# Performance work log

Measured on AMD Instinct MI355X. Metric: run time of the kernel, lower is better.

The kernel has to match this reference:

```python
import jax, jax.numpy as jnp
import numpy as np

N, IN_SZ, OUT_SZ = 8192, 512, 64

def setup_inputs() -> dict:
    key = jax.random.key(0)
    ks = jax.random.split(key, 7)
    s_in = 1.0 / np.sqrt(IN_SZ)
    inp = {
        "input": jax.random.normal(ks[0], (N, IN_SZ), dtype=jnp.float32),
        "Wq": jax.random.uniform(ks[1], (OUT_SZ, IN_SZ), jnp.float32, -s_in, s_in),
        "bq": jax.random.uniform(ks[2], (OUT_SZ,), jnp.float32, -s_in, s_in),
        "Wk": jax.random.uniform(ks[3], (OUT_SZ, IN_SZ), jnp.float32, -s_in, s_in),
        "bk": jax.random.uniform(ks[4], (OUT_SZ,), jnp.float32, -s_in, s_in),
        "Wv": jax.random.uniform(ks[5], (OUT_SZ, IN_SZ), jnp.float32, -s_in, s_in),
        "bv": jax.random.uniform(ks[6], (OUT_SZ,), jnp.float32, -s_in, s_in),
    }
    return inp

def reference(input, Wq, bq, Wk, bk, Wv, bv):
    # torch nn.Linear: x @ W.T + b
    q = input @ Wq.T + bq  # [N, out]
    k = input @ Wk.T + bk  # [N, out]
    v = input @ Wv.T + bv  # [N, out]
    # NOTE: original module has NO 1/sqrt(d) scaling.
    scores = jax.nn.softmax(q @ k.T, axis=-1)  # [N, N]
    return scores @ v  # [N, out]
```

## Files before the change

kernel.cpp:

```cpp
#include <hip/hip_runtime.h>
#include <math.h>

#define SA_N   8192
#define SA_IN  512
#define SA_D   64
#define G_SPL  16

typedef short s16x8 __attribute__((ext_vector_type(8)));
typedef float f32x16 __attribute__((ext_vector_type(16)));

#define MFMA32(A, B, C) __builtin_amdgcn_mfma_f32_32x32x16_bf16((A), (B), (C), 0, 0, 0)

static __device__ __forceinline__ unsigned short f2bf_rn(float x) {
    unsigned int u = __float_as_uint(x);
    unsigned int r = (u + 0x7FFFu + ((u >> 16) & 1u)) >> 16;
    return (unsigned short)r;
}

static __device__ __forceinline__ void trunc_split(float f, unsigned short* hi, unsigned short* lo) {
    unsigned int u = __float_as_uint(f);
    *hi = (unsigned short)(u >> 16);
    float lf = f - __uint_as_float(u & 0xFFFF0000u);
    *lo = (unsigned short)(__float_as_uint(lf) >> 16);
}

static __device__ __forceinline__ void split8(const float4 a, const float4 b, s16x8* xh, s16x8* xl) {
    union { unsigned int u[4]; s16x8 v; } H, L;
    const float f[8] = {a.x, a.y, a.z, a.w, b.x, b.y, b.z, b.w};
#pragma unroll
    for (int p = 0; p < 4; ++p) {
        const unsigned int u0 = __float_as_uint(f[2 * p]);
        const unsigned int u1 = __float_as_uint(f[2 * p + 1]);
        H.u[p] = (u0 >> 16) | (u1 & 0xFFFF0000u);
        const float l0 = f[2 * p]     - __uint_as_float(u0 & 0xFFFF0000u);
        const float l1 = f[2 * p + 1] - __uint_as_float(u1 & 0xFFFF0000u);
        L.u[p] = (__float_as_uint(l0) >> 16) | (__float_as_uint(l1) & 0xFFFF0000u);
    }
    *xh = H.v; *xl = L.v;
}

static __device__ __forceinline__ s16x8 pack_rn8(const float4 a, const float4 b) {
    union { unsigned int u[4]; s16x8 v; } P;
    const float f[8] = {a.x, a.y, a.z, a.w, b.x, b.y, b.z, b.w};
#pragma unroll
    for (int p = 0; p < 4; ++p)
        P.u[p] = (unsigned int)f2bf_rn(f[2 * p]) | ((unsigned int)f2bf_rn(f[2 * p + 1]) << 16);
    return P.v;
}

__global__ __launch_bounds__(256, 2) void qkv_kernel(
    const float* __restrict__ in,
    const float* __restrict__ Wq, const float* __restrict__ bq,
    const float* __restrict__ Wk, const float* __restrict__ bk,
    const float* __restrict__ Wv, const float* __restrict__ bv,
    unsigned short* __restrict__ Qhi, unsigned short* __restrict__ Qlo,
    unsigned short* __restrict__ KhiF, unsigned short* __restrict__ KloF,
    unsigned short* __restrict__ VF)
{
    __shared__ float cbuf[2][4][64][20];
    __shared__ __align__(16) unsigned short stage[4096];
    const int t    = threadIdx.x;
    const int w    = t >> 6;
    const int lane = t & 63;
    const int h    = lane >> 5;
    const int q32  = lane & 31;
    const int mat  = blockIdx.x >> 8;
    const int jt   = blockIdx.x & 255;
    const int rows0 = jt * 32;

    const float* W = (mat == 0) ? Wq : (mat == 1 ? Wk : Wv);
    const float* B = (mat == 0) ? bq : (mat == 1 ? bk : bv);

    f32x16 accA[2] = {};
    f32x16 accB[2] = {};

#pragma unroll 2
    for (int ksl = 0; ksl < 8; ++ksl) {
        const int ks = (w << 3) + ksl;
        const float* xp = in + (size_t)(rows0 + q32) * SA_IN + ks * 16 + h * 8;
        const float4 xa = *(const float4*)xp;
        const float4 xb = *(const float4*)(xp + 4);
        s16x8 xh, xl;
        split8(xa, xb, &xh, &xl);
#pragma unroll
        for (int mt = 0; mt < 2; ++mt) {
            const float* wp = W + (size_t)(mt * 32 + q32) * SA_IN + ks * 16 + h * 8;
            const float4 wa = *(const float4*)wp;
            const float4 wb = *(const float4*)(wp + 4);
            if (mat < 2) {
                s16x8 ah, al;
                split8(wa, wb, &ah, &al);
                accA[mt] = MFMA32(ah, xh, accA[mt]);
                accB[mt] = MFMA32(ah, xl, accB[mt]);
                accA[mt] = MFMA32(al, xh, accA[mt]);
            } else {
                const s16x8 ah = pack_rn8(wa, wb);
                accA[mt] = MFMA32(ah, xh, accA[mt]);
            }
        }
    }

#pragma unroll
    for (int mt = 0; mt < 2; ++mt) {
        f32x16 tot = accA[mt];
        if (mat < 2) {
#pragma unroll
            for (int r = 0; r < 16; ++r) tot[r] += accB[mt][r];
        }
#pragma unroll
        for (int rg = 0; rg < 4; ++rg) {
            float4 vv = { tot[4 * rg + 0], tot[4 * rg + 1],
                          tot[4 * rg + 2], tot[4 * rg + 3] };
            *(float4*)&cbuf[mt][w][lane][4 * rg] = vv;
        }
    }
    __syncthreads();
    if (w < 2) {
        const int mt = w;
        float c[16];
#pragma unroll
        for (int rg = 0; rg < 4; ++rg) {
            const float4 s0 = *(const float4*)&cbuf[mt][0][lane][4 * rg];
            const float4 s1 = *(const float4*)&cbuf[mt][1][lane][4 * rg];
            const float4 s2 = *(const float4*)&cbuf[mt][2][lane][4 * rg];
            const float4 s3 = *(const float4*)&cbuf[mt][3][lane][4 * rg];
            c[4 * rg + 0] = (s0.x + s1.x) + (s2.x + s3.x);
            c[4 * rg + 1] = (s0.y + s1.y) + (s2.y + s3.y);
            c[4 * rg + 2] = (s0.z + s1.z) + (s2.z + s3.z);
            c[4 * rg + 3] = (s0.w + s1.w) + (s2.w + s3.w);
        }
#pragma unroll
        for (int r = 0; r < 16; ++r) {
            const int o = mt * 32 + (r & 3) + 8 * (r >> 2) + 4 * h;
            const float val = c[r] + B[o];
            if (mat == 0) {
                unsigned short hi, lo;
                trunc_split(val, &hi, &lo);
                stage[q32 * 64 + o]        = hi;
                stage[2048 + q32 * 64 + o] = lo;
            } else if (mat == 1) {
                unsigned short hi, lo;
                trunc_split(val, &hi, &lo);
                const int kl_ = ((o >> 4) * 64 + ((o >> 3) & 1) * 32 + q32) * 8 + (o & 7);
                stage[kl_]        = hi;
                stage[2048 + kl_] = lo;
            } else {
                const int vl_ = ((o >> 5) * 2 + ((q32 >> 4) & 1)) * 512
                              + ((q32 >> 3) & 1) * 256 + (o & 31) * 8 + (q32 & 7);
                stage[vl_] = f2bf_rn(val);
            }
        }
    }
    __syncthreads();

    {
        const uint4* st4 = (const uint4*)stage;
        if (mat == 0) {
            for (int i = t; i < 512; i += 256) {
                unsigned short* dst = ((i < 256) ? Qhi : Qlo) + (size_t)rows0 * 64 + (i & 255) * 8;
                *(uint4*)dst = st4[i];
            }
        } else if (mat == 1) {
            for (int i = t; i < 512; i += 256) {
                unsigned short* dst = ((i < 256) ? KhiF : KloF) + (size_t)jt * 2048 + (i & 255) * 8;
                *(uint4*)dst = st4[i];
            }
        } else {
            *(uint4*)(VF + (size_t)jt * 2048 + t * 8) = st4[t];
        }
    }
}

__global__ __launch_bounds__(256, 2) void attn_kernel(
    const unsigned short* __restrict__ Qhi, const unsigned short* __restrict__ Qlo,
    const unsigned short* __restrict__ KhiF, const unsigned short* __restrict__ KloF,
    const unsigned short* __restrict__ VF,
    unsigned short* __restrict__ Opart, float* __restrict__ Lpart)
{
    const int t    = threadIdx.x;
    const int w    = t >> 6;
    const int lane = t & 63;
    const int h    = lane >> 5;
    const int q32  = lane & 31;
    const int qb   = blockIdx.x >> 4;
    const int g    = blockIdx.x & 15;
    const int q0   = (qb * 4 + w) * 32;

    s16x8 qh[4], ql[4];
#pragma unroll
    for (int s = 0; s < 4; ++s) {
        const size_t off = (size_t)(q0 + q32) * 64 + s * 16 + h * 8;
        qh[s] = *reinterpret_cast<const s16x8*>(Qhi + off);
        ql[s] = *reinterpret_cast<const s16x8*>(Qlo + off);
    }

    const s16x8* KH = reinterpret_cast<const s16x8*>(KhiF);
    const s16x8* KL = reinterpret_cast<const s16x8*>(KloF);
    const s16x8* VV = reinterpret_cast<const s16x8*>(VF);

    f32x16 O0 = {}, O1 = {};
    float lsum = 0.f;

    auto process = [&](const s16x8* kh, const s16x8* kl, const s16x8* vv) {
        f32x16 Sa = {}, Sb = {}, Sc = {};
#pragma unroll
        for (int s = 0; s < 4; ++s) {
            Sa = MFMA32(kh[s], qh[s], Sa);
            Sb = MFMA32(kh[s], ql[s], Sb);
            Sc = MFMA32(kl[s], qh[s], Sc);
        }

        float e[16];
#pragma unroll
        for (int r = 0; r < 16; ++r) e[r] = __expf((Sa[r] + Sb[r]) + Sc[r]);
        lsum += (((e[0] + e[1]) + (e[2] + e[3])) + ((e[4] + e[5]) + (e[6] + e[7])))
              + (((e[8] + e[9]) + (e[10] + e[11])) + ((e[12] + e[13]) + (e[14] + e[15])));

        unsigned int pk[8];
#pragma unroll
        for (int j2 = 0; j2 < 8; ++j2)
            pk[j2] = (__float_as_uint(e[2 * j2]) >> 16) | (__float_as_uint(e[2 * j2 + 1]) & 0xFFFF0000u);

        unsigned int x[8];
#pragma unroll
        for (int j2 = 0; j2 < 8; ++j2) x[j2] = (unsigned int)__shfl_xor((int)pk[j2], 32, 64);

        union { unsigned int u[4]; s16x8 v; } P0, P1;
        P0.u[0] = h ? x[2]  : pk[0];
        P0.u[1] = h ? x[3]  : pk[1];
        P0.u[2] = h ? pk[2] : x[0];
        P0.u[3] = h ? pk[3] : x[1];
        P1.u[0] = h ? x[6]  : pk[4];
        P1.u[1] = h ? x[7]  : pk[5];
        P1.u[2] = h ? pk[6] : x[4];
        P1.u[3] = h ? pk[7] : x[5];

        O0 = MFMA32(vv[0], P0.v, O0);
        O0 = MFMA32(vv[1], P1.v, O0);
        O1 = MFMA32(vv[2], P0.v, O1);
        O1 = MFMA32(vv[3], P1.v, O1);
    };

    for (int it = 0; it < 16; it += 2) {
        const int jtA = g * 16 + it;
        const int jtB = jtA + 1;
        s16x8 khA[4], klA[4], vA[4], khB[4], klB[4], vB[4];
#pragma unroll
        for (int s = 0; s < 4; ++s) {
            khA[s] = KH[(jtA * 4 + s) * 64 + lane];
            klA[s] = KL[(jtA * 4 + s) * 64 + lane];
            vA[s]  = VV[(jtA * 4 + s) * 64 + lane];
            khB[s] = KH[(jtB * 4 + s) * 64 + lane];
            klB[s] = KL[(jtB * 4 + s) * 64 + lane];
            vB[s]  = VV[(jtB * 4 + s) * 64 + lane];
        }
        process(khA, klA, vA);
        process(khB, klB, vB);
    }

    lsum += __shfl_xor(lsum, 32, 64);

    const size_t qg = (size_t)g * SA_N + q0 + q32;
#pragma unroll
    for (int rg = 0; rg < 4; ++rg) {
        const int d0 = 8 * rg + 4 * h;
        uint2 s0, s1;
        s0.x = (unsigned int)f2bf_rn(O0[4 * rg + 0]) | ((unsigned int)f2bf_rn(O0[4 * rg + 1]) << 16);
        s0.y = (unsigned int)f2bf_rn(O0[4 * rg + 2]) | ((unsigned int)f2bf_rn(O0[4 * rg + 3]) << 16);
        s1.x = (unsigned int)f2bf_rn(O1[4 * rg + 0]) | ((unsigned int)f2bf_rn(O1[4 * rg + 1]) << 16);
        s1.y = (unsigned int)f2bf_rn(O1[4 * rg + 2]) | ((unsigned int)f2bf_rn(O1[4 * rg + 3]) << 16);
        *(uint2*)(Opart + qg * 64 + d0)      = s0;
        *(uint2*)(Opart + qg * 64 + d0 + 32) = s1;
    }
    if (h == 0) Lpart[qg] = lsum;
}

__global__ __launch_bounds__(256) void combine_kernel(
    const unsigned short* __restrict__ Opart, const float* __restrict__ Lpart,
    float* __restrict__ out)
{
    const int tid = blockIdx.x * 256 + threadIdx.x;
    const int q  = tid >> 5;
    const int dp = tid & 31;
    const unsigned int* OP = (const unsigned int*)Opart;
    float s0 = 0.f, s1 = 0.f, lt = 0.f;
#pragma unroll
    for (int g = 0; g < G_SPL; ++g) {
        const unsigned int v = OP[((size_t)g * SA_N + q) * 32 + dp];
        s0 += __uint_as_float(v << 16);
        s1 += __uint_as_float(v & 0xFFFF0000u);
        lt += Lpart[(size_t)g * SA_N + q];
    }
    float2 r = { s0 / lt, s1 / lt };
    *(float2*)&out[(size_t)q * 64 + dp * 2] = r;
}

extern "C" void kernel_launch(void* const* d_in, const int* in_sizes, int n_in,
                              void* d_out, int out_size, void* d_ws, size_t ws_size,
                              hipStream_t stream) {
    const float* input = (const float*)d_in[0];
    const float* Wq    = (const float*)d_in[1];
    const float* bq    = (const float*)d_in[2];
    const float* Wk    = (const float*)d_in[3];
    const float* bk    = (const float*)d_in[4];
    const float* Wv    = (const float*)d_in[5];
    const float* bv    = (const float*)d_in[6];
    float* out = (float*)d_out;

    const size_t SEG = (size_t)SA_N * 64;
    unsigned short* Qhi  = (unsigned short*)d_ws;
    unsigned short* Qlo  = Qhi  + SEG;
    unsigned short* KhiF = Qlo  + SEG;
    unsigned short* KloF = KhiF + SEG;
    unsigned short* VF   = KloF + SEG;
    unsigned short* Opart = VF  + SEG;
    float*          Lpart = (float*)(Opart + (size_t)G_SPL * SA_N * 64);

    qkv_kernel<<<768, 256, 0, stream>>>(input, Wq, bq, Wk, bk, Wv, bv,
                                        Qhi, Qlo, KhiF, KloF, VF);
    attn_kernel<<<64 * G_SPL, 256, 0, stream>>>(Qhi, Qlo, KhiF, KloF, VF, Opart, Lpart);
    combine_kernel<<<1024, 256, 0, stream>>>(Opart, Lpart, out);
}
```

Baseline: 146.9 us.

## Fuse combine into attention via last-block counter, use exp2 and perm packing

Removes the separate combine kernel. The last of the 16 split blocks per query block, found through an atomic counter reset in the QKV kernel, reduces the partial outputs and sums itself. Q is pre-scaled by log2(e) so the softmax can use the hardware exp2 directly. The three score MFMA chains are merged into one accumulator, and the bf16 hi-half packing now uses v_perm. This saves a launch and some ALU work, but the final reduction now runs on only 64 blocks at the tail of the attention kernel, and the single accumulator chain serializes the MFMAs.

Measured after the change: 340.2 us. 2.32x slower.

```diff
diff --git a/kernel.cpp b/kernel.cpp
--- a/kernel.cpp
+++ b/kernel.cpp
@@ -5,6 +5,7 @@
 #define SA_IN  512
 #define SA_D   64
 #define G_SPL  16
+#define LOG2E  1.44269504f
 
 typedef short s16x8 __attribute__((ext_vector_type(8)));
 typedef float f32x16 __attribute__((ext_vector_type(16)));
@@ -24,6 +25,10 @@
     *lo = (unsigned short)(__float_as_uint(lf) >> 16);
 }
 
+static __device__ __forceinline__ unsigned int pack_hi16(unsigned int u0, unsigned int u1) {
+    return __builtin_amdgcn_perm(u1, u0, 0x07060302u);
+}
+
 static __device__ __forceinline__ void split8(const float4 a, const float4 b, s16x8* xh, s16x8* xl) {
     union { unsigned int u[4]; s16x8 v; } H, L;
     const float f[8] = {a.x, a.y, a.z, a.w, b.x, b.y, b.z, b.w};
@@ -31,10 +36,10 @@
     for (int p = 0; p < 4; ++p) {
         const unsigned int u0 = __float_as_uint(f[2 * p]);
         const unsigned int u1 = __float_as_uint(f[2 * p + 1]);
-        H.u[p] = (u0 >> 16) | (u1 & 0xFFFF0000u);
+        H.u[p] = pack_hi16(u0, u1);
         const float l0 = f[2 * p]     - __uint_as_float(u0 & 0xFFFF0000u);
         const float l1 = f[2 * p + 1] - __uint_as_float(u1 & 0xFFFF0000u);
-        L.u[p] = (__float_as_uint(l0) >> 16) | (__float_as_uint(l1) & 0xFFFF0000u);
+        L.u[p] = pack_hi16(__float_as_uint(l0), __float_as_uint(l1));
     }
     *xh = H.v; *xl = L.v;
 }
@@ -55,7 +60,7 @@
     const float* __restrict__ Wv, const float* __restrict__ bv,
     unsigned short* __restrict__ Qhi, unsigned short* __restrict__ Qlo,
     unsigned short* __restrict__ KhiF, unsigned short* __restrict__ KloF,
-    unsigned short* __restrict__ VF)
+    unsigned short* __restrict__ VF, unsigned int* __restrict__ cnt)
 {
     __shared__ float cbuf[2][4][64][20];
     __shared__ __align__(16) unsigned short stage[4096];
@@ -67,6 +72,8 @@
     const int mat  = blockIdx.x >> 8;
     const int jt   = blockIdx.x & 255;
     const int rows0 = jt * 32;
+
+    if (blockIdx.x == 0 && t < 64) cnt[t] = 0;
 
     const float* W = (mat == 0) ? Wq : (mat == 1 ? Wk : Wv);
     const float* B = (mat == 0) ? bq : (mat == 1 ? bk : bv);
@@ -132,8 +139,9 @@
 #pragma unroll
         for (int r = 0; r < 16; ++r) {
             const int o = mt * 32 + (r & 3) + 8 * (r >> 2) + 4 * h;
-            const float val = c[r] + B[o];
+            float val = c[r] + B[o];
             if (mat == 0) {
+                val *= LOG2E;
                 unsigned short hi, lo;
                 trunc_split(val, &hi, &lo);
                 stage[q32 * 64 + o]        = hi;
@@ -175,8 +183,10 @@
     const unsigned short* __restrict__ Qhi, const unsigned short* __restrict__ Qlo,
     const unsigned short* __restrict__ KhiF, const unsigned short* __restrict__ KloF,
     const unsigned short* __restrict__ VF,
-    unsigned short* __restrict__ Opart, float* __restrict__ Lpart)
+    unsigned short* __restrict__ Opart, float* __restrict__ Lpart,
+    unsigned int* __restrict__ cnt, float* __restrict__ out)
 {
+    __shared__ int is_last;
     const int t    = threadIdx.x;
     const int w    = t >> 6;
     const int lane = t & 63;
@@ -202,24 +212,24 @@
     float lsum = 0.f;
 
     auto process = [&](const s16x8* kh, const s16x8* kl, const s16x8* vv) {
-        f32x16 Sa = {}, Sb = {}, Sc = {};
-#pragma unroll
-        for (int s = 0; s < 4; ++s) {
-            Sa = MFMA32(kh[s], qh[s], Sa);
-            Sb = MFMA32(kh[s], ql[s], Sb);
-            Sc = MFMA32(kl[s], qh[s], Sc);
-        }
+        f32x16 S = {};
+#pragma unroll
+        for (int s = 0; s < 4; ++s) S = MFMA32(kh[s], qh[s], S);
+#pragma unroll
+        for (int s = 0; s < 4; ++s) S = MFMA32(kh[s], ql[s], S);
+#pragma unroll
+        for (int s = 0; s < 4; ++s) S = MFMA32(kl[s], qh[s], S);
 
         float e[16];
 #pragma unroll
-        for (int r = 0; r < 16; ++r) e[r] = __expf((Sa[r] + Sb[r]) + Sc[r]);
+        for (int r = 0; r < 16; ++r) e[r] = __builtin_amdgcn_exp2f(S[r]);
         lsum += (((e[0] + e[1]) + (e[2] + e[3])) + ((e[4] + e[5]) + (e[6] + e[7])))
               + (((e[8] + e[9]) + (e[10] + e[11])) + ((e[12] + e[13]) + (e[14] + e[15])));
 
         unsigned int pk[8];
 #pragma unroll
         for (int j2 = 0; j2 < 8; ++j2)
-            pk[j2] = (__float_as_uint(e[2 * j2]) >> 16) | (__float_as_uint(e[2 * j2 + 1]) & 0xFFFF0000u);
+            pk[j2] = pack_hi16(__float_as_uint(e[2 * j2]), __float_as_uint(e[2 * j2 + 1]));
 
         unsigned int x[8];
 #pragma unroll
@@ -273,26 +283,33 @@
         *(uint2*)(Opart + qg * 64 + d0 + 32) = s1;
     }
     if (h == 0) Lpart[qg] = lsum;
-}
-
-__global__ __launch_bounds__(256) void combine_kernel(
-    const unsigned short* __restrict__ Opart, const float* __restrict__ Lpart,
-    float* __restrict__ out)
-{
-    const int tid = blockIdx.x * 256 + threadIdx.x;
-    const int q  = tid >> 5;
-    const int dp = tid & 31;
-    const unsigned int* OP = (const unsigned int*)Opart;
-    float s0 = 0.f, s1 = 0.f, lt = 0.f;
-#pragma unroll
-    for (int g = 0; g < G_SPL; ++g) {
-        const unsigned int v = OP[((size_t)g * SA_N + q) * 32 + dp];
-        s0 += __uint_as_float(v << 16);
-        s1 += __uint_as_float(v & 0xFFFF0000u);
-        lt += Lpart[(size_t)g * SA_N + q];
-    }
-    float2 r = { s0 / lt, s1 / lt };
-    *(float2*)&out[(size_t)q * 64 + dp * 2] = r;
+
+    __threadfence();
+    __syncthreads();
+    if (t == 0) {
+        const unsigned int old = atomicAdd(&cnt[qb], 1u);
+        is_last = (old == (unsigned int)(G_SPL - 1));
+    }
+    __syncthreads();
+    if (is_last) {
+        __threadfence();
+        const unsigned int* OP = (const unsigned int*)Opart;
+        for (int i = t; i < 128 * 32; i += 256) {
+            const int qlcl = i >> 5;
+            const int dp   = i & 31;
+            const int q    = qb * 128 + qlcl;
+            float s0 = 0.f, s1 = 0.f, lt = 0.f;
+#pragma unroll
+            for (int gg = 0; gg < G_SPL; ++gg) {
+                const unsigned int v = OP[((size_t)gg * SA_N + q) * 32 + dp];
+                s0 += __uint_as_float(v << 16);
+                s1 += __uint_as_float(v & 0xFFFF0000u);
+                lt += Lpart[(size_t)gg * SA_N + q];
+            }
+            float2 r = { s0 / lt, s1 / lt };
+            *(float2*)&out[(size_t)q * 64 + dp * 2] = r;
+        }
+    }
 }
 
 extern "C" void kernel_launch(void* const* d_in, const int* in_sizes, int n_in,
@@ -315,9 +332,10 @@
     unsigned short* VF   = KloF + SEG;
     unsigned short* Opart = VF  + SEG;
     float*          Lpart = (float*)(Opart + (size_t)G_SPL * SA_N * 64);
+    unsigned int*   cnt   = (unsigned int*)(Lpart + (size_t)G_SPL * SA_N);
 
     qkv_kernel<<<768, 256, 0, stream>>>(input, Wq, bq, Wk, bk, Wv, bv,
-                                        Qhi, Qlo, KhiF, KloF, VF);
-    attn_kernel<<<64 * G_SPL, 256, 0, stream>>>(Qhi, Qlo, KhiF, KloF, VF, Opart, Lpart);
-    combine_kernel<<<1024, 256, 0, stream>>>(Opart, Lpart, out);
-}
+                                        Qhi, Qlo, KhiF, KloF, VF, cnt);
+    attn_kernel<<<64 * G_SPL, 256, 0, stream>>>(Qhi, Qlo, KhiF, KloF, VF,
+                                                Opart, Lpart, cnt, out);
+}
```
